# Optimization experiments

Measured on AMD Instinct MI355X. Metric: run time of the kernel, lower is better.

Reference implementation:

```python
import jax, jax.numpy as jnp
import numpy as np

GROUPS = 32
EPS = 1e-5
NUM_HEADS = 8


def group_norm(x, w, b):
    # x: (B, C, H, W)
    B, C, H, W = x.shape
    xg = x.reshape(B, GROUPS, C // GROUPS, H, W)
    mean = xg.mean(axis=(2, 3, 4), keepdims=True)
    var = xg.var(axis=(2, 3, 4), keepdims=True)
    xg = (xg - mean) * jax.lax.rsqrt(var + EPS)
    x = xg.reshape(B, C, H, W)
    return x * w[None, :, None, None] + b[None, :, None, None]


def setup_inputs() -> dict:
    key = jax.random.key(0)
    ks = jax.random.split(key, 4)
    B, C, H, W = 16, 512, 32, 32
    x = jax.random.normal(ks[0], (B, C, H, W), dtype=jnp.float32)
    gn_w = jnp.ones((C,), dtype=jnp.float32)
    gn_b = jnp.zeros((C,), dtype=jnp.float32)
    qkv_w = jax.random.normal(ks[1], (3 * C, C), dtype=jnp.float32) * 0.02  # 1x1 conv, no bias
    proj_w = jax.random.normal(ks[2], (C, C), dtype=jnp.float32) * 0.02     # 1x1 conv
    proj_b = jax.random.normal(ks[3], (C,), dtype=jnp.float32) * 0.02
    return {"x": x, "gn_w": gn_w, "gn_b": gn_b, "qkv_w": qkv_w,
            "proj_w": proj_w, "proj_b": proj_b}


def reference(x, gn_w, gn_b, qkv_w, proj_w, proj_b):
    B, C, H, W = x.shape
    heads = NUM_HEADS
    head_dim = C // heads
    HW = H * W
    scale = 1.0 / (head_dim ** 0.5)

    x = group_norm(x, gn_w, gn_b)  # residual uses the NORMED x, matching source

    qkv = jnp.einsum('bchw,oc->bohw', x, qkv_w)                     # (B, 3C, H, W)
    qkv = qkv.reshape(B, 3, heads, head_dim, HW)
    q, k, v = qkv[:, 0], qkv[:, 1], qkv[:, 2]                       # (B, heads, head_dim, HW)

    # Replicate the source's exact permute(0,2,3,1)+reshape (scrambles semantics, but faithful)
    def to_bmh(t):
        return jnp.transpose(t, (0, 2, 3, 1)).reshape(B * heads, HW, head_dim)
    q, k, v = to_bmh(q), to_bmh(k), to_bmh(v)

    attn = jax.nn.softmax(jnp.einsum('bnd,bmd->bnm', q, k) * scale, axis=-1)  # (B*heads, HW, HW)
    h = jnp.einsum('bnm,bmd->bnd', attn, v)                                   # (B*heads, HW, head_dim)

    h = h.reshape(B, heads, H, W, head_dim)
    h = jnp.transpose(h, (0, 1, 4, 2, 3)).reshape(B, C, H, W)

    out = jnp.einsum('bchw,oc->bohw', h, proj_w) + proj_b[None, :, None, None]
    return out + x
```

## Files before the change

### kernel.cpp

```cpp
#include <hip/hip_runtime.h>
#include <stdint.h>

typedef unsigned short u16;
typedef short bfrag __attribute__((ext_vector_type(8)));
typedef float ffrag __attribute__((ext_vector_type(4)));
typedef u16 us4 __attribute__((ext_vector_type(4)));
typedef uint32_t u32x4 __attribute__((ext_vector_type(4)));

#define HW 1024
#define C_DIM 512
#define O3 1536
#define BATCH 16

__device__ __forceinline__ u16 f2bf(float f) {
    uint32_t u = __builtin_bit_cast(uint32_t, f);
    u += 0x7FFFu + ((u >> 16) & 1u);
    return (u16)(u >> 16);
}
__device__ __forceinline__ float bf2f(u16 v) {
    return __builtin_bit_cast(float, (uint32_t)v << 16);
}
__device__ __forceinline__ float fexp2(float x) { return __builtin_amdgcn_exp2f(x); }
__device__ __forceinline__ void async16(const u16* src, u16* ldsDst) {
    __builtin_amdgcn_global_load_lds(
        (const __attribute__((address_space(1))) uint32_t*)src,
        (__attribute__((address_space(3))) uint32_t*)ldsDst, 16, 0, 0);
}

__global__ __launch_bounds__(256) void gn_cvt_kernel(
    const float* __restrict__ x, const float* __restrict__ gw, const float* __restrict__ gb,
    u16* __restrict__ xgt,
    const float* __restrict__ qkvw, u16* __restrict__ qkvwb,
    const float* __restrict__ projw, u16* __restrict__ projwb)
{
    __shared__ u16 tile[16 * 1032];
    __shared__ float red[8];
    const int tid = threadIdx.x;
    if (blockIdx.x >= 512) {
        int i = (blockIdx.x - 512) * 256 + tid;
        if (i < 196608) {
            float4 v = ((const float4*)qkvw)[i];
            us4 o = { f2bf(v.x), f2bf(v.y), f2bf(v.z), f2bf(v.w) };
            ((us4*)qkvwb)[i] = o;
        } else {
            int j = i - 196608;
            float4 v = ((const float4*)projw)[j];
            us4 o = { f2bf(v.x), f2bf(v.y), f2bf(v.z), f2bf(v.w) };
            ((us4*)projwb)[j] = o;
        }
        return;
    }
    const int batch = blockIdx.x >> 5, g = blockIdx.x & 31;
    const float* xp = x + ((size_t)batch * C_DIM + g * 16) * HW;

    float s = 0.f, ss = 0.f;
#pragma unroll
    for (int it = 0; it < 16; ++it) {
        int i4 = it * 256 + tid;
        float4 v = ((const float4*)xp)[i4];
        int ci = i4 >> 8;
        int hw = (i4 & 255) * 4;
        s += v.x + v.y + v.z + v.w;
        ss += v.x * v.x + v.y * v.y + v.z * v.z + v.w * v.w;
        us4 u = { f2bf(v.x), f2bf(v.y), f2bf(v.z), f2bf(v.w) };
        *(us4*)&tile[ci * 1032 + hw] = u;
    }
#pragma unroll
    for (int m = 1; m <= 32; m <<= 1) { s += __shfl_xor(s, m, 64); ss += __shfl_xor(ss, m, 64); }
    if ((tid & 63) == 0) { red[tid >> 6] = s; red[4 + (tid >> 6)] = ss; }
    __syncthreads();
    float S = red[0] + red[1] + red[2] + red[3];
    float SS = red[4] + red[5] + red[6] + red[7];
    const float mean = S * (1.f / 16384.f);
    const float istd = rsqrtf(SS * (1.f / 16384.f) - mean * mean + 1e-5f);

    u16* xtp = xgt + (size_t)batch * HW * C_DIM + g * 16;
#pragma unroll
    for (int it = 0; it < 16; ++it) {
        int hw = (tid >> 2) + it * 64;
        int c0 = (tid & 3) * 4;
        us4 o;
#pragma unroll
        for (int k2 = 0; k2 < 4; ++k2) {
            int ci = c0 + k2;
            float sc = gw[g * 16 + ci] * istd;
            float bi = gb[g * 16 + ci] - mean * sc;
            o[k2] = f2bf(bf2f(tile[ci * 1032 + hw]) * sc + bi);
        }
        *(us4*)&xtp[(size_t)hw * C_DIM + c0] = o;
    }
}

__global__ __launch_bounds__(256, 2) void qkv_gemm_kernel(
    const u16* __restrict__ A, const u16* __restrict__ B, u16* __restrict__ Out,
    u16* __restrict__ vtout)
{
    __shared__ __align__(16) u16 smem[24576];
    const int tid = threadIdx.x;
    const int l = tid & 63, w = tid >> 6;
    const int swz = (blockIdx.x & 7) * 96 + (blockIdx.x >> 3);
    const int batch = swz / 48, t = swz % 48;
    const int tm = t / 12, tn = t % 12;
    A += (size_t)batch * (HW * C_DIM) + (size_t)tm * 256 * 512;
    B += (size_t)tn * 128 * 512;

    auto stageA = [&](u16* lds, int kt) {
#pragma unroll
        for (int i = 0; i < 4; ++i) {
            int L = i * 256 + tid;
            int row = L >> 2, cs = L & 3;
            int c = cs ^ ((row & 3) ^ ((row >> 2) & 3));
            async16(A + (size_t)row * 512 + kt * 32 + c * 8,
                    lds + (size_t)(i * 256 + (tid & 192)) * 8);
        }
    };
    auto stageB = [&](u16* lds, int kt) {
#pragma unroll
        for (int i = 0; i < 2; ++i) {
            int L = i * 256 + tid;
            int row = L >> 2, cs = L & 3;
            int c = cs ^ ((row & 3) ^ ((row >> 2) & 3));
            async16(B + (size_t)row * 512 + kt * 32 + c * 8,
                    lds + (size_t)(i * 256 + (tid & 192)) * 8);
        }
    };

    ffrag acc[8][4] = {};
    stageA(smem, 0); stageB(smem + 16384, 0);
    const int wm = (w >> 1) * 128, wn = (w & 1) * 64;
#pragma unroll
    for (int kt = 0; kt < 16; ++kt) {
        const int cur = kt & 1;
        asm volatile("s_waitcnt vmcnt(0)" ::: "memory");
        __builtin_amdgcn_s_barrier();
        __builtin_amdgcn_sched_barrier(0);
        if (kt < 15) {
            stageA(smem + (cur ^ 1) * 8192, kt + 1);
            stageB(smem + 16384 + (cur ^ 1) * 4096, kt + 1);
        }
        const u16* As = smem + cur * 8192;
        const u16* Bs = smem + 16384 + cur * 4096;
        bfrag a[8], bb[4];
#pragma unroll
        for (int j = 0; j < 4; ++j) {
            int col = wn + j * 16 + (l & 15);
            int ch2 = (l >> 4) ^ ((col & 3) ^ ((col >> 2) & 3));
            bb[j] = *(const bfrag*)&Bs[col * 32 + ch2 * 8];
        }
#pragma unroll
        for (int i = 0; i < 8; ++i) {
            int row = wm + i * 16 + (l & 15);
            int ch = (l >> 4) ^ ((row & 3) ^ ((row >> 2) & 3));
            a[i] = *(const bfrag*)&As[row * 32 + ch * 8];
        }
        __builtin_amdgcn_s_setprio(1);
#pragma unroll
        for (int i = 0; i < 8; ++i)
#pragma unroll
            for (int j = 0; j < 4; ++j)
                acc[i][j] = __builtin_amdgcn_mfma_f32_16x16x32_bf16(a[i], bb[j], acc[i][j], 0, 0, 0);
        __builtin_amdgcn_s_setprio(0);
    }
    __syncthreads();
    const int rbase = tm * 256 + wm + ((l >> 4) << 2);
    const int cbase = tn * 128 + wn + (l & 15);
    if (tn < 8) {
        u16* outp = Out + (size_t)batch * (HW * O3);
#pragma unroll
        for (int i = 0; i < 8; ++i)
#pragma unroll
            for (int j = 0; j < 4; ++j)
#pragma unroll
                for (int r = 0; r < 4; ++r)
                    outp[(size_t)(rbase + i * 16 + r) * O3 + cbase + j * 16] = f2bf(acc[i][j][r]);
    } else {
        u16* vb = vtout + (size_t)batch * 8 * 64 * HW;
        const int hd0 = tn * 128 - 1024;
#pragma unroll
        for (int h2 = 0; h2 < 2; ++h2) {
            if ((w >> 1) == h2) {
#pragma unroll
                for (int i = 0; i < 8; ++i)
#pragma unroll
                    for (int j = 0; j < 4; ++j) {
                        int hd_l = wn + (l & 15) + j * 16;
                        int m_l = wm + i * 16 + ((l >> 4) << 2);
                        int s_l = (m_l & ~31) | ((m_l & 12) << 1) | ((m_l & 16) >> 2) | (m_l & 3);
                        int c4 = (s_l & 127) >> 2;
                        int c4s = c4 ^ (hd_l & 31);
                        us4 pk = { f2bf(acc[i][j][0]), f2bf(acc[i][j][1]),
                                   f2bf(acc[i][j][2]), f2bf(acc[i][j][3]) };
                        *(us4*)&smem[hd_l * 128 + c4s * 4] = pk;
                    }
            }
            __syncthreads();
#pragma unroll
            for (int it = 0; it < 16; ++it) {
                int f4 = it * 256 + tid;
                int hd_l = f4 >> 5, c4 = f4 & 31;
                int c4s = c4 ^ (hd_l & 31);
                us4 v = *(const us4*)&smem[hd_l * 128 + c4s * 4];
                *(us4*)&vb[(size_t)(hd0 + hd_l) * HW + tm * 256 + h2 * 128 + c4 * 4] = v;
            }
            __syncthreads();
        }
    }
}

__global__ __launch_bounds__(256) void proj_gemm_kernel(
    const u16* __restrict__ A, const u16* __restrict__ B, float* __restrict__ Out,
    const float* __restrict__ bias, const u16* __restrict__ residT)
{
    __shared__ __align__(16) u16 smem[24576];
    const int tid = threadIdx.x;
    const int l = tid & 63, w = tid >> 6;
    const int swz = (blockIdx.x & 7) * 64 + (blockIdx.x >> 3);
    const int batch = swz / 32, t = swz % 32;
    const int tm = t / 8, tn = t % 8;
    A += (size_t)tm * 128 * 512;
    B += (size_t)batch * (HW * C_DIM) + (size_t)tn * 128 * 512;

    auto stage = [&](const u16* gbase, u16* lds, int kt) {
#pragma unroll
        for (int i = 0; i < 2; ++i) {
            int L = i * 256 + tid;
            int row = L >> 2, cs = L & 3;
            int c = cs ^ ((row & 3) ^ ((row >> 2) & 3));
            async16(gbase + (size_t)row * 512 + kt * 32 + c * 8,
                    lds + (size_t)(i * 256 + (tid & 192)) * 8);
        }
    };

    ffrag acc[4][4] = {};
    stage(A, smem, 0);        stage(B, smem + 12288, 0);
    stage(A, smem + 4096, 1); stage(B, smem + 16384, 1);
    const int wr = (w >> 1) * 64, wc = (w & 1) * 64;
#pragma unroll
    for (int kt = 0; kt < 16; ++kt) {
        const int cur = kt % 3;
        if (kt < 15) asm volatile("s_waitcnt vmcnt(4)" ::: "memory");
        else         asm volatile("s_waitcnt vmcnt(0)" ::: "memory");
        __builtin_amdgcn_s_barrier();
        __builtin_amdgcn_sched_barrier(0);
        if (kt < 14) {
            int nxt = (kt + 2) % 3;
            stage(A, smem + nxt * 4096, kt + 2);
            stage(B, smem + 12288 + nxt * 4096, kt + 2);
        }
        const u16* As = smem + cur * 4096;
        const u16* Bs = smem + 12288 + cur * 4096;
        bfrag a[4], bb[4];
#pragma unroll
        for (int i = 0; i < 4; ++i) {
            int row = wr + i * 16 + (l & 15);
            int ch = (l >> 4) ^ ((row & 3) ^ ((row >> 2) & 3));
            a[i] = *(const bfrag*)&As[row * 32 + ch * 8];
            int col = wc + i * 16 + (l & 15);
            int ch2 = (l >> 4) ^ ((col & 3) ^ ((col >> 2) & 3));
            bb[i] = *(const bfrag*)&Bs[col * 32 + ch2 * 8];
        }
        __builtin_amdgcn_s_setprio(1);
#pragma unroll
        for (int i = 0; i < 4; ++i)
#pragma unroll
            for (int j = 0; j < 4; ++j)
                acc[i][j] = __builtin_amdgcn_mfma_f32_16x16x32_bf16(a[i], bb[j], acc[i][j], 0, 0, 0);
        __builtin_amdgcn_s_setprio(0);
    }
    const int rbase = tm * 128 + wr + ((l >> 4) << 2);
    const int cbase = tn * 128 + wc + (l & 15);
    float* outp = Out + (size_t)batch * (C_DIM * HW);
    const u16* rt = residT + (size_t)batch * (HW * C_DIM);
#pragma unroll
    for (int i = 0; i < 4; ++i)
#pragma unroll
        for (int j = 0; j < 4; ++j) {
            int cc = cbase + j * 16;
            us4 rv = *(const us4*)&rt[(size_t)cc * C_DIM + rbase + i * 16];
#pragma unroll
            for (int r = 0; r < 4; ++r) {
                int rr = rbase + i * 16 + r;
                outp[(size_t)rr * HW + cc] = acc[i][j][r] + bias[rr] + bf2f(rv[r]);
            }
        }
}

__global__ __launch_bounds__(512, 4) void attn_kernel(const u16* __restrict__ qkvt,
                                                      const u16* __restrict__ vt,
                                                      u16* __restrict__ ht)
{
    __shared__ __align__(16) u16 KVs[6 * 4096];
    const int tid = threadIdx.x, l = tid & 63, w = tid >> 6, g = l >> 4;
    const int swz = ((blockIdx.x & 7) << 6) + (blockIdx.x >> 3);
    const int nt = swz & 3, h = (swz >> 2) & 7, batch = swz >> 5;
    const u16* Qb = qkvt + (size_t)batch * HW * O3 + h * 64;
    const u16* Kb = Qb + 512;
    const u16* Vtb = vt + (size_t)(batch * 8 + h) * 64 * HW;
    const int n0 = nt * 256 + w * 32;
    const float cexp = 0.125f * 1.44269504f;

    bfrag qf[2][2];
#pragma unroll
    for (int ni = 0; ni < 2; ++ni)
#pragma unroll
        for (int kc = 0; kc < 2; ++kc)
            qf[ni][kc] = *(const bfrag*)&Qb[(size_t)(n0 + ni * 16 + (l & 15)) * O3 + kc * 32 + g * 8];

    bfrag ones;
#pragma unroll
    for (int k = 0; k < 8; ++k) ones[k] = (short)0x3F80;

    auto stageK = [&](int ms, u16* lds) {
        int row = tid >> 3, c = (tid & 7) ^ (row & 7);
        async16(&Kb[(size_t)(ms * 64 + row) * O3 + c * 8], lds + (size_t)(tid & 448) * 8);
    };
    auto stageV = [&](int ms, u16* lds) {
        int row = tid >> 3, c = (tid & 7) ^ (row & 7);
        async16(&Vtb[(size_t)row * HW + ms * 64 + c * 8], lds + (size_t)(tid & 448) * 8);
    };

    ffrag hacc[2][4] = {};
    ffrag accl[2] = {};

    stageK(0, KVs);        stageV(0, KVs + 3 * 4096);
    stageK(1, KVs + 4096); stageV(1, KVs + 4 * 4096);

#pragma unroll
    for (int ms = 0; ms < 16; ++ms) {
        const int cur = ms % 3;
        const u16* Ksc = KVs + cur * 4096;
        const u16* Vsc = KVs + (3 + cur) * 4096;
        if (ms < 15) asm volatile("s_waitcnt vmcnt(2)" ::: "memory");
        else         asm volatile("s_waitcnt vmcnt(0)" ::: "memory");
        __builtin_amdgcn_s_barrier();
        __builtin_amdgcn_sched_barrier(0);
        if (ms < 14) {
            int nxt = (ms + 2) % 3;
            stageK(ms + 2, KVs + nxt * 4096);
            stageV(ms + 2, KVs + (3 + nxt) * 4096);
        }

        ffrag s[2][4] = {};
        __builtin_amdgcn_s_setprio(1);
#pragma unroll
        for (int mj = 0; mj < 4; ++mj)
#pragma unroll
            for (int kc = 0; kc < 2; ++kc) {
                int m = mj * 16 + (l & 15);
                int ch = (kc * 4 + g) ^ (m & 7);
                bfrag kf = *(const bfrag*)&Ksc[m * 64 + ch * 8];
#pragma unroll
                for (int ni = 0; ni < 2; ++ni)
                    s[ni][mj] = __builtin_amdgcn_mfma_f32_16x16x32_bf16(kf, qf[ni][kc], s[ni][mj], 0, 0, 0);
            }
        __builtin_amdgcn_s_setprio(0);

        u32x4 pk[2][2];
#pragma unroll
        for (int ni = 0; ni < 2; ++ni)
#pragma unroll
            for (int kc = 0; kc < 2; ++kc)
#pragma unroll
                for (int hh = 0; hh < 2; ++hh) {
                    int mj = kc * 2 + hh;
                    float p0 = fexp2(s[ni][mj][0] * cexp);
                    float p1 = fexp2(s[ni][mj][1] * cexp);
                    float p2 = fexp2(s[ni][mj][2] * cexp);
                    float p3 = fexp2(s[ni][mj][3] * cexp);
                    pk[ni][kc][hh * 2] = __builtin_amdgcn_perm(
                        __builtin_bit_cast(uint32_t, p1), __builtin_bit_cast(uint32_t, p0), 0x07060302u);
                    pk[ni][kc][hh * 2 + 1] = __builtin_amdgcn_perm(
                        __builtin_bit_cast(uint32_t, p3), __builtin_bit_cast(uint32_t, p2), 0x07060302u);
                }

        __builtin_amdgcn_s_setprio(1);
#pragma unroll
        for (int kc = 0; kc < 2; ++kc) {
            bfrag pf0 = __builtin_bit_cast(bfrag, pk[0][kc]);
            bfrag pf1 = __builtin_bit_cast(bfrag, pk[1][kc]);
            accl[0] = __builtin_amdgcn_mfma_f32_16x16x32_bf16(pf0, ones, accl[0], 0, 0, 0);
            accl[1] = __builtin_amdgcn_mfma_f32_16x16x32_bf16(pf1, ones, accl[1], 0, 0, 0);
#pragma unroll
            for (int dj = 0; dj < 4; ++dj) {
                int d = dj * 16 + (l & 15);
                int ch = (kc * 4 + g) ^ (d & 7);
                bfrag vf = *(const bfrag*)&Vsc[d * 64 + ch * 8];
                hacc[0][dj] = __builtin_amdgcn_mfma_f32_16x16x32_bf16(pf0, vf, hacc[0][dj], 0, 0, 0);
                hacc[1][dj] = __builtin_amdgcn_mfma_f32_16x16x32_bf16(pf1, vf, hacc[1][dj], 0, 0, 0);
            }
        }
        __builtin_amdgcn_s_setprio(0);
    }

    u16* hp = ht + (size_t)batch * HW * C_DIM + h * 64;
#pragma unroll
    for (int ni = 0; ni < 2; ++ni) {
        float linv[4];
#pragma unroll
        for (int r = 0; r < 4; ++r) linv[r] = __builtin_amdgcn_rcpf(accl[ni][r]);
#pragma unroll
        for (int dj = 0; dj < 4; ++dj)
#pragma unroll
            for (int r = 0; r < 4; ++r) {
                int n = n0 + ni * 16 + g * 4 + r;
                int d = dj * 16 + (l & 15);
                hp[(size_t)n * C_DIM + d] = f2bf(hacc[ni][dj][r] * linv[r]);
            }
    }
}

extern "C" void kernel_launch(void* const* d_in, const int* in_sizes, int n_in,
                              void* d_out, int out_size, void* d_ws, size_t ws_size,
                              hipStream_t stream)
{
    const float* x = (const float*)d_in[0];
    const float* gw = (const float*)d_in[1];
    const float* gb = (const float*)d_in[2];
    const float* qkvw = (const float*)d_in[3];
    const float* projw = (const float*)d_in[4];
    const float* projb = (const float*)d_in[5];
    float* out = (float*)d_out;
    char* ws = (char*)d_ws;
    u16* ht    = (u16*)(ws);
    u16* xgt   = (u16*)(ws + 16777216);
    u16* qkvt  = (u16*)(ws + 33554432);
    u16* vt    = (u16*)(ws + 83886080);
    u16* qkvwb = (u16*)(ws + 100663296);
    u16* projwb= (u16*)(ws + 102236160);

    gn_cvt_kernel<<<1536, 256, 0, stream>>>(x, gw, gb, xgt, qkvw, qkvwb, projw, projwb);
    qkv_gemm_kernel<<<768, 256, 0, stream>>>(xgt, qkvwb, qkvt, vt);
    attn_kernel<<<512, 512, 0, stream>>>(qkvt, vt, ht);
    proj_gemm_kernel<<<512, 256, 0, stream>>>(projwb, ht, out, projb, xgt);
}
```

Before: 108.3 us.

## Shrink QKV tile with triple-buffered loads and stage epilogue stores through LDS

The QKV GEMM tile drops from 256x128 to 128x128, doubling the grid, and switches to a 3-stage cp.async-style pipeline that waits with vmcnt(4) instead of draining every iteration. The QKV, projection and attention epilogues now write results into LDS first and then emit coalesced 8/16-byte global stores, replacing scattered 2- and 4-byte per-element stores. This targets uncoalesced write traffic and load latency, at the cost of extra barriers and LDS round trips. The smaller tile also means more global reloads of the weight operand.

```diff
diff --git a/kernel.cpp b/kernel.cpp
--- a/kernel.cpp
+++ b/kernel.cpp
@@ -91,118 +91,111 @@
     }
 }
 
-__global__ __launch_bounds__(256, 2) void qkv_gemm_kernel(
+__global__ __launch_bounds__(256) void qkv_gemm_kernel(
     const u16* __restrict__ A, const u16* __restrict__ B, u16* __restrict__ Out,
     u16* __restrict__ vtout)
 {
     __shared__ __align__(16) u16 smem[24576];
     const int tid = threadIdx.x;
     const int l = tid & 63, w = tid >> 6;
-    const int swz = (blockIdx.x & 7) * 96 + (blockIdx.x >> 3);
-    const int batch = swz / 48, t = swz % 48;
+    const int swz = (blockIdx.x & 7) * 192 + (blockIdx.x >> 3);
+    const int batch = swz / 96, t = swz % 96;
     const int tm = t / 12, tn = t % 12;
-    A += (size_t)batch * (HW * C_DIM) + (size_t)tm * 256 * 512;
+    A += (size_t)batch * (HW * C_DIM) + (size_t)tm * 128 * 512;
     B += (size_t)tn * 128 * 512;
 
-    auto stageA = [&](u16* lds, int kt) {
-#pragma unroll
-        for (int i = 0; i < 4; ++i) {
-            int L = i * 256 + tid;
-            int row = L >> 2, cs = L & 3;
-            int c = cs ^ ((row & 3) ^ ((row >> 2) & 3));
-            async16(A + (size_t)row * 512 + kt * 32 + c * 8,
-                    lds + (size_t)(i * 256 + (tid & 192)) * 8);
-        }
-    };
-    auto stageB = [&](u16* lds, int kt) {
+    auto stage = [&](const u16* gbase, u16* lds, int kt) {
 #pragma unroll
         for (int i = 0; i < 2; ++i) {
             int L = i * 256 + tid;
             int row = L >> 2, cs = L & 3;
             int c = cs ^ ((row & 3) ^ ((row >> 2) & 3));
-            async16(B + (size_t)row * 512 + kt * 32 + c * 8,
+            async16(gbase + (size_t)row * 512 + kt * 32 + c * 8,
                     lds + (size_t)(i * 256 + (tid & 192)) * 8);
         }
     };
 
-    ffrag acc[8][4] = {};
-    stageA(smem, 0); stageB(smem + 16384, 0);
-    const int wm = (w >> 1) * 128, wn = (w & 1) * 64;
+    ffrag acc[4][4] = {};
+    stage(A, smem, 0);        stage(B, smem + 12288, 0);
+    stage(A, smem + 4096, 1); stage(B, smem + 16384, 1);
+    const int wr = (w >> 1) * 64, wc = (w & 1) * 64;
 #pragma unroll
     for (int kt = 0; kt < 16; ++kt) {
-        const int cur = kt & 1;
-        asm volatile("s_waitcnt vmcnt(0)" ::: "memory");
+        const int cur = kt % 3;
+        if (kt < 15) asm volatile("s_waitcnt vmcnt(4)" ::: "memory");
+        else         asm volatile("s_waitcnt vmcnt(0)" ::: "memory");
         __builtin_amdgcn_s_barrier();
         __builtin_amdgcn_sched_barrier(0);
-        if (kt < 15) {
-            stageA(smem + (cur ^ 1) * 8192, kt + 1);
-            stageB(smem + 16384 + (cur ^ 1) * 4096, kt + 1);
-        }
-        const u16* As = smem + cur * 8192;
-        const u16* Bs = smem + 16384 + cur * 4096;
-        bfrag a[8], bb[4];
-#pragma unroll
-        for (int j = 0; j < 4; ++j) {
-            int col = wn + j * 16 + (l & 15);
-            int ch2 = (l >> 4) ^ ((col & 3) ^ ((col >> 2) & 3));
-            bb[j] = *(const bfrag*)&Bs[col * 32 + ch2 * 8];
-        }
-#pragma unroll
-        for (int i = 0; i < 8; ++i) {
-            int row = wm + i * 16 + (l & 15);
+        if (kt < 14) {
+            int nxt = (kt + 2) % 3;
+            stage(A, smem + nxt * 4096, kt + 2);
+            stage(B, smem + 12288 + nxt * 4096, kt + 2);
+        }
+        const u16* As = smem + cur * 4096;
+        const u16* Bs = smem + 12288 + cur * 4096;
+        bfrag a[4], bb[4];
+#pragma unroll
+        for (int i = 0; i < 4; ++i) {
+            int row = wr + i * 16 + (l & 15);
             int ch = (l >> 4) ^ ((row & 3) ^ ((row >> 2) & 3));
             a[i] = *(const bfrag*)&As[row * 32 + ch * 8];
+            int col = wc + i * 16 + (l & 15);
+            int ch2 = (l >> 4) ^ ((col & 3) ^ ((col >> 2) & 3));
+            bb[i] = *(const bfrag*)&Bs[col * 32 + ch2 * 8];
         }
         __builtin_amdgcn_s_setprio(1);
 #pragma unroll
-        for (int i = 0; i < 8; ++i)
+        for (int i = 0; i < 4; ++i)
 #pragma unroll
             for (int j = 0; j < 4; ++j)
                 acc[i][j] = __builtin_amdgcn_mfma_f32_16x16x32_bf16(a[i], bb[j], acc[i][j], 0, 0, 0);
         __builtin_amdgcn_s_setprio(0);
     }
     __syncthreads();
-    const int rbase = tm * 256 + wm + ((l >> 4) << 2);
-    const int cbase = tn * 128 + wn + (l & 15);
     if (tn < 8) {
+#pragma unroll
+        for (int i = 0; i < 4; ++i)
+#pragma unroll
+            for (int j = 0; j < 4; ++j) {
+                int row_l = wr + i * 16 + ((l >> 4) << 2);
+                int col_l = wc + j * 16 + (l & 15);
+#pragma unroll
+                for (int r = 0; r < 4; ++r)
+                    smem[(row_l + r) * 136 + col_l] = f2bf(acc[i][j][r]);
+            }
+        __syncthreads();
         u16* outp = Out + (size_t)batch * (HW * O3);
 #pragma unroll
-        for (int i = 0; i < 8; ++i)
-#pragma unroll
-            for (int j = 0; j < 4; ++j)
-#pragma unroll
-                for (int r = 0; r < 4; ++r)
-                    outp[(size_t)(rbase + i * 16 + r) * O3 + cbase + j * 16] = f2bf(acc[i][j][r]);
+        for (int it = 0; it < 16; ++it) {
+            int f = it * 256 + tid;
+            int row_l = f >> 5, o4 = f & 31;
+            *(us4*)&outp[(size_t)(tm * 128 + row_l) * O3 + tn * 128 + o4 * 4] =
+                *(const us4*)&smem[row_l * 136 + o4 * 4];
+        }
     } else {
         u16* vb = vtout + (size_t)batch * 8 * 64 * HW;
         const int hd0 = tn * 128 - 1024;
 #pragma unroll
-        for (int h2 = 0; h2 < 2; ++h2) {
-            if ((w >> 1) == h2) {
-#pragma unroll
-                for (int i = 0; i < 8; ++i)
-#pragma unroll
-                    for (int j = 0; j < 4; ++j) {
-                        int hd_l = wn + (l & 15) + j * 16;
-                        int m_l = wm + i * 16 + ((l >> 4) << 2);
-                        int s_l = (m_l & ~31) | ((m_l & 12) << 1) | ((m_l & 16) >> 2) | (m_l & 3);
-                        int c4 = (s_l & 127) >> 2;
-                        int c4s = c4 ^ (hd_l & 31);
-                        us4 pk = { f2bf(acc[i][j][0]), f2bf(acc[i][j][1]),
-                                   f2bf(acc[i][j][2]), f2bf(acc[i][j][3]) };
-                        *(us4*)&smem[hd_l * 128 + c4s * 4] = pk;
-                    }
+        for (int i = 0; i < 4; ++i)
+#pragma unroll
+            for (int j = 0; j < 4; ++j) {
+                int hd_l = wc + (l & 15) + j * 16;
+                int m_l = wr + i * 16 + ((l >> 4) << 2);
+                int s_l = (m_l & 96) | ((m_l & 12) << 1) | ((m_l & 16) >> 2);
+                int c4 = s_l >> 2;
+                int c4s = c4 ^ (hd_l & 7);
+                us4 pk = { f2bf(acc[i][j][0]), f2bf(acc[i][j][1]),
+                           f2bf(acc[i][j][2]), f2bf(acc[i][j][3]) };
+                *(us4*)&smem[hd_l * 128 + c4s * 4] = pk;
             }
-            __syncthreads();
-#pragma unroll
-            for (int it = 0; it < 16; ++it) {
-                int f4 = it * 256 + tid;
-                int hd_l = f4 >> 5, c4 = f4 & 31;
-                int c4s = c4 ^ (hd_l & 31);
-                us4 v = *(const us4*)&smem[hd_l * 128 + c4s * 4];
-                *(us4*)&vb[(size_t)(hd0 + hd_l) * HW + tm * 256 + h2 * 128 + c4 * 4] = v;
-            }
-            __syncthreads();
+        __syncthreads();
+#pragma unroll
+        for (int it = 0; it < 16; ++it) {
+            int f4 = it * 256 + tid;
+            int hd_l = f4 >> 5, c4 = f4 & 31;
+            int c4s = c4 ^ (hd_l & 7);
+            us4 v = *(const us4*)&smem[hd_l * 128 + c4s * 4];
+            *(us4*)&vb[(size_t)(hd0 + hd_l) * HW + tm * 128 + c4 * 4] = v;
         }
     }
 }
@@ -267,22 +260,39 @@
                 acc[i][j] = __builtin_amdgcn_mfma_f32_16x16x32_bf16(a[i], bb[j], acc[i][j], 0, 0, 0);
         __builtin_amdgcn_s_setprio(0);
     }
+    __syncthreads();
     const int rbase = tm * 128 + wr + ((l >> 4) << 2);
     const int cbase = tn * 128 + wc + (l & 15);
     float* outp = Out + (size_t)batch * (C_DIM * HW);
     const u16* rt = residT + (size_t)batch * (HW * C_DIM);
-#pragma unroll
-    for (int i = 0; i < 4; ++i)
-#pragma unroll
-        for (int j = 0; j < 4; ++j) {
-            int cc = cbase + j * 16;
-            us4 rv = *(const us4*)&rt[(size_t)cc * C_DIM + rbase + i * 16];
-#pragma unroll
-            for (int r = 0; r < 4; ++r) {
-                int rr = rbase + i * 16 + r;
-                outp[(size_t)rr * HW + cc] = acc[i][j][r] + bias[rr] + bf2f(rv[r]);
-            }
-        }
+    float* lf = (float*)smem;
+#pragma unroll
+    for (int h2 = 0; h2 < 2; ++h2) {
+        if ((w >> 1) == h2) {
+#pragma unroll
+            for (int i = 0; i < 4; ++i)
+#pragma unroll
+                for (int j = 0; j < 4; ++j) {
+                    int cc = cbase + j * 16;
+                    us4 rv = *(const us4*)&rt[(size_t)cc * C_DIM + rbase + i * 16];
+                    int row_h = i * 16 + ((l >> 4) << 2);
+                    int col_l = wc + j * 16 + (l & 15);
+#pragma unroll
+                    for (int r = 0; r < 4; ++r)
+                        lf[(row_h + r) * 132 + col_l] =
+                            acc[i][j][r] + bias[rbase + i * 16 + r] + bf2f(rv[r]);
+                }
+        }
+        __syncthreads();
+#pragma unroll
+        for (int it = 0; it < 8; ++it) {
+            int f = it * 256 + tid;
+            int row_l = f >> 5, c4 = f & 31;
+            float4 v = *(const float4*)&lf[row_l * 132 + c4 * 4];
+            *(float4*)&outp[(size_t)(tm * 128 + h2 * 64 + row_l) * HW + tn * 128 + c4 * 4] = v;
+        }
+        __syncthreads();
+    }
 }
 
 __global__ __launch_bounds__(512, 4) void attn_kernel(const u16* __restrict__ qkvt,
@@ -392,20 +402,29 @@
         __builtin_amdgcn_s_setprio(0);
     }
 
-    u16* hp = ht + (size_t)batch * HW * C_DIM + h * 64;
+    __syncthreads();
 #pragma unroll
     for (int ni = 0; ni < 2; ++ni) {
         float linv[4];
 #pragma unroll
         for (int r = 0; r < 4; ++r) linv[r] = __builtin_amdgcn_rcpf(accl[ni][r]);
 #pragma unroll
-        for (int dj = 0; dj < 4; ++dj)
-#pragma unroll
-            for (int r = 0; r < 4; ++r) {
-                int n = n0 + ni * 16 + g * 4 + r;
-                int d = dj * 16 + (l & 15);
-                hp[(size_t)n * C_DIM + d] = f2bf(hacc[ni][dj][r] * linv[r]);
-            }
+        for (int dj = 0; dj < 4; ++dj) {
+            int n_l = w * 32 + ni * 16 + g * 4;
+            int d = dj * 16 + (l & 15);
+#pragma unroll
+            for (int r = 0; r < 4; ++r)
+                KVs[(n_l + r) * 68 + d] = f2bf(hacc[ni][dj][r] * linv[r]);
+        }
+    }
+    __syncthreads();
+    u16* hp = ht + (size_t)batch * HW * C_DIM + h * 64;
+#pragma unroll
+    for (int it = 0; it < 8; ++it) {
+        int f = it * 512 + tid;
+        int n_l = f >> 4, d4 = f & 15;
+        us4 v = *(const us4*)&KVs[n_l * 68 + d4 * 4];
+        *(us4*)&hp[(size_t)(nt * 256 + n_l) * C_DIM + d4 * 4] = v;
     }
 }
 
@@ -429,7 +448,7 @@
     u16* projwb= (u16*)(ws + 102236160);
 
     gn_cvt_kernel<<<1536, 256, 0, stream>>>(x, gw, gb, xgt, qkvw, qkvwb, projw, projwb);
-    qkv_gemm_kernel<<<768, 256, 0, stream>>>(xgt, qkvwb, qkvt, vt);
+    qkv_gemm_kernel<<<1536, 256, 0, stream>>>(xgt, qkvwb, qkvt, vt);
     attn_kernel<<<512, 512, 0, stream>>>(qkvt, vt, ht);
     proj_gemm_kernel<<<512, 256, 0, stream>>>(projwb, ht, out, projb, xgt);
 }
```

Measured after the change: 109.3 us. No clear change (+0.9%).

## Retile QKV GEMM to 128x128 blocks with 64-deep K steps

Applied to the files above, without the earlier changes.

The QKV projection GEMM moves from 256x128 output tiles with K=32 per stage to 128x128 tiles with K=64 per stage, doubling the grid to 1536 blocks. LDS swizzling becomes an 8-chunk XOR, and the V-transpose epilogue is simplified to a single pass. This is meant to raise parallelism and halve the number of barrier-synchronised K iterations, at the cost of less operand reuse per block and more global traffic for the A and B tiles.

```diff
diff --git a/kernel.cpp b/kernel.cpp
--- a/kernel.cpp
+++ b/kernel.cpp
@@ -91,83 +91,73 @@
     }
 }
 
-__global__ __launch_bounds__(256, 2) void qkv_gemm_kernel(
+__global__ __launch_bounds__(256) void qkv_gemm_kernel(
     const u16* __restrict__ A, const u16* __restrict__ B, u16* __restrict__ Out,
     u16* __restrict__ vtout)
 {
-    __shared__ __align__(16) u16 smem[24576];
+    __shared__ __align__(16) u16 smem[32768];
     const int tid = threadIdx.x;
     const int l = tid & 63, w = tid >> 6;
-    const int swz = (blockIdx.x & 7) * 96 + (blockIdx.x >> 3);
-    const int batch = swz / 48, t = swz % 48;
+    const int swz = (blockIdx.x & 7) * 192 + (blockIdx.x >> 3);
+    const int batch = swz / 96, t = swz % 96;
     const int tm = t / 12, tn = t % 12;
-    A += (size_t)batch * (HW * C_DIM) + (size_t)tm * 256 * 512;
+    A += (size_t)batch * (HW * C_DIM) + (size_t)tm * 128 * 512;
     B += (size_t)tn * 128 * 512;
 
-    auto stageA = [&](u16* lds, int kt) {
+    auto stage = [&](const u16* gbase, u16* lds, int kt) {
 #pragma unroll
         for (int i = 0; i < 4; ++i) {
             int L = i * 256 + tid;
-            int row = L >> 2, cs = L & 3;
-            int c = cs ^ ((row & 3) ^ ((row >> 2) & 3));
-            async16(A + (size_t)row * 512 + kt * 32 + c * 8,
+            int row = L >> 3, cs = L & 7;
+            int c = cs ^ (row & 7);
+            async16(gbase + (size_t)row * 512 + kt * 64 + c * 8,
                     lds + (size_t)(i * 256 + (tid & 192)) * 8);
         }
     };
-    auto stageB = [&](u16* lds, int kt) {
-#pragma unroll
-        for (int i = 0; i < 2; ++i) {
-            int L = i * 256 + tid;
-            int row = L >> 2, cs = L & 3;
-            int c = cs ^ ((row & 3) ^ ((row >> 2) & 3));
-            async16(B + (size_t)row * 512 + kt * 32 + c * 8,
-                    lds + (size_t)(i * 256 + (tid & 192)) * 8);
-        }
-    };
-
-    ffrag acc[8][4] = {};
-    stageA(smem, 0); stageB(smem + 16384, 0);
-    const int wm = (w >> 1) * 128, wn = (w & 1) * 64;
-#pragma unroll
-    for (int kt = 0; kt < 16; ++kt) {
+
+    ffrag acc[4][4] = {};
+    stage(A, smem, 0); stage(B, smem + 16384, 0);
+    const int wr = (w >> 1) * 64, wc = (w & 1) * 64;
+#pragma unroll
+    for (int kt = 0; kt < 8; ++kt) {
         const int cur = kt & 1;
         asm volatile("s_waitcnt vmcnt(0)" ::: "memory");
         __builtin_amdgcn_s_barrier();
         __builtin_amdgcn_sched_barrier(0);
-        if (kt < 15) {
-            stageA(smem + (cur ^ 1) * 8192, kt + 1);
-            stageB(smem + 16384 + (cur ^ 1) * 4096, kt + 1);
+        if (kt < 7) {
+            stage(A, smem + (cur ^ 1) * 8192, kt + 1);
+            stage(B, smem + 16384 + (cur ^ 1) * 8192, kt + 1);
         }
         const u16* As = smem + cur * 8192;
-        const u16* Bs = smem + 16384 + cur * 4096;
-        bfrag a[8], bb[4];
-#pragma unroll
-        for (int j = 0; j < 4; ++j) {
-            int col = wn + j * 16 + (l & 15);
-            int ch2 = (l >> 4) ^ ((col & 3) ^ ((col >> 2) & 3));
-            bb[j] = *(const bfrag*)&Bs[col * 32 + ch2 * 8];
-        }
-#pragma unroll
-        for (int i = 0; i < 8; ++i) {
-            int row = wm + i * 16 + (l & 15);
-            int ch = (l >> 4) ^ ((row & 3) ^ ((row >> 2) & 3));
-            a[i] = *(const bfrag*)&As[row * 32 + ch * 8];
-        }
-        __builtin_amdgcn_s_setprio(1);
-#pragma unroll
-        for (int i = 0; i < 8; ++i)
-#pragma unroll
-            for (int j = 0; j < 4; ++j)
-                acc[i][j] = __builtin_amdgcn_mfma_f32_16x16x32_bf16(a[i], bb[j], acc[i][j], 0, 0, 0);
-        __builtin_amdgcn_s_setprio(0);
+        const u16* Bs = smem + 16384 + cur * 8192;
+#pragma unroll
+        for (int kc = 0; kc < 2; ++kc) {
+            bfrag a[4], bb[4];
+#pragma unroll
+            for (int i = 0; i < 4; ++i) {
+                int row = wr + i * 16 + (l & 15);
+                int ch = (kc * 4 + (l >> 4)) ^ (row & 7);
+                a[i] = *(const bfrag*)&As[row * 64 + ch * 8];
+                int col = wc + i * 16 + (l & 15);
+                int ch2 = (kc * 4 + (l >> 4)) ^ (col & 7);
+                bb[i] = *(const bfrag*)&Bs[col * 64 + ch2 * 8];
+            }
+            __builtin_amdgcn_s_setprio(1);
+#pragma unroll
+            for (int i = 0; i < 4; ++i)
+#pragma unroll
+                for (int j = 0; j < 4; ++j)
+                    acc[i][j] = __builtin_amdgcn_mfma_f32_16x16x32_bf16(a[i], bb[j], acc[i][j], 0, 0, 0);
+            __builtin_amdgcn_s_setprio(0);
+        }
     }
     __syncthreads();
-    const int rbase = tm * 256 + wm + ((l >> 4) << 2);
-    const int cbase = tn * 128 + wn + (l & 15);
+    const int rbase = tm * 128 + wr + ((l >> 4) << 2);
+    const int cbase = tn * 128 + wc + (l & 15);
     if (tn < 8) {
         u16* outp = Out + (size_t)batch * (HW * O3);
 #pragma unroll
-        for (int i = 0; i < 8; ++i)
+        for (int i = 0; i < 4; ++i)
 #pragma unroll
             for (int j = 0; j < 4; ++j)
 #pragma unroll
@@ -177,32 +167,26 @@
         u16* vb = vtout + (size_t)batch * 8 * 64 * HW;
         const int hd0 = tn * 128 - 1024;
 #pragma unroll
-        for (int h2 = 0; h2 < 2; ++h2) {
-            if ((w >> 1) == h2) {
-#pragma unroll
-                for (int i = 0; i < 8; ++i)
-#pragma unroll
-                    for (int j = 0; j < 4; ++j) {
-                        int hd_l = wn + (l & 15) + j * 16;
-                        int m_l = wm + i * 16 + ((l >> 4) << 2);
-                        int s_l = (m_l & ~31) | ((m_l & 12) << 1) | ((m_l & 16) >> 2) | (m_l & 3);
-                        int c4 = (s_l & 127) >> 2;
-                        int c4s = c4 ^ (hd_l & 31);
-                        us4 pk = { f2bf(acc[i][j][0]), f2bf(acc[i][j][1]),
-                                   f2bf(acc[i][j][2]), f2bf(acc[i][j][3]) };
-                        *(us4*)&smem[hd_l * 128 + c4s * 4] = pk;
-                    }
-            }
-            __syncthreads();
-#pragma unroll
-            for (int it = 0; it < 16; ++it) {
-                int f4 = it * 256 + tid;
-                int hd_l = f4 >> 5, c4 = f4 & 31;
-                int c4s = c4 ^ (hd_l & 31);
-                us4 v = *(const us4*)&smem[hd_l * 128 + c4s * 4];
-                *(us4*)&vb[(size_t)(hd0 + hd_l) * HW + tm * 256 + h2 * 128 + c4 * 4] = v;
-            }
-            __syncthreads();
+        for (int i = 0; i < 4; ++i)
+#pragma unroll
+            for (int j = 0; j < 4; ++j) {
+                int hd_l = wc + (l & 15) + j * 16;
+                int m_l = wr + i * 16 + ((l >> 4) << 2);
+                int s_l = (m_l & 96) | ((m_l & 12) << 1) | ((m_l & 16) >> 2);
+                int c4 = s_l >> 2;
+                int c4s = c4 ^ (hd_l & 7);
+                us4 pk = { f2bf(acc[i][j][0]), f2bf(acc[i][j][1]),
+                           f2bf(acc[i][j][2]), f2bf(acc[i][j][3]) };
+                *(us4*)&smem[hd_l * 128 + c4s * 4] = pk;
+            }
+        __syncthreads();
+#pragma unroll
+        for (int it = 0; it < 16; ++it) {
+            int f4 = it * 256 + tid;
+            int hd_l = f4 >> 5, c4 = f4 & 31;
+            int c4s = c4 ^ (hd_l & 7);
+            us4 v = *(const us4*)&smem[hd_l * 128 + c4s * 4];
+            *(us4*)&vb[(size_t)(hd0 + hd_l) * HW + tm * 128 + c4 * 4] = v;
         }
     }
 }
@@ -429,7 +413,7 @@
     u16* projwb= (u16*)(ws + 102236160);
 
     gn_cvt_kernel<<<1536, 256, 0, stream>>>(x, gw, gb, xgt, qkvw, qkvwb, projw, projwb);
-    qkv_gemm_kernel<<<768, 256, 0, stream>>>(xgt, qkvwb, qkvt, vt);
+    qkv_gemm_kernel<<<1536, 256, 0, stream>>>(xgt, qkvwb, qkvt, vt);
     attn_kernel<<<512, 512, 0, stream>>>(qkvt, vt, ht);
     proj_gemm_kernel<<<512, 256, 0, stream>>>(projwb, ht, out, projb, xgt);
 }
```

Measured after the change: 103.7 us. 4.2% less time.
